# Kernel tuning notes

Hardware: AMD Instinct MI355X
Metric: run time of the kernel (lower is better)

Reference implementation:

```python
import jax, jax.numpy as jnp
import numpy as np

FIELD_DIMS = [26000] * 39
EMBED_DIM = 64
MLP_DIMS = [400, 400, 400]
BATCH = 16384
OFFSETS = jnp.asarray(np.concatenate(([0], np.cumsum(FIELD_DIMS)[:-1])), dtype=jnp.int32)
BN_INV = 1.0 / np.sqrt(1.0 + 1e-5)  # eval-mode BatchNorm1d: running_mean=0, running_var=1


def setup_inputs() -> dict:
    key = jax.random.key(0)
    ks = jax.random.split(key, 16)
    B, F, E = BATCH, len(FIELD_DIMS), EMBED_DIM
    V = sum(FIELD_DIMS)
    s = lambda k, shp, sc=0.05: (jax.random.normal(k, shp, jnp.float32) * sc)
    inp = {
        "x": jax.random.randint(ks[0], (B, F), 0, FIELD_DIMS[0], dtype=jnp.int32),
        "emb_table": s(ks[1], (V, E)),
        "lin_table": s(ks[2], (V, 1)),
        "lin_bias": jnp.zeros((1,), jnp.float32),
        "sparse_var": s(ks[3], (F, E), 0.1),
        "Wt": s(ks[4], (F, E, E)),  # per-field Linear weights, (out,in) layout
        "bt": jnp.zeros((F, E), jnp.float32),
    }
    dims = [F * E] + MLP_DIMS
    for i in range(3):
        inp[f"W{i+1}"] = s(ks[5 + i], (dims[i], dims[i + 1]))
        inp[f"b{i+1}"] = jnp.zeros((dims[i + 1],), jnp.float32)
        inp[f"g{i+1}"] = jnp.ones((dims[i + 1],), jnp.float32)
        inp[f"be{i+1}"] = jnp.zeros((dims[i + 1],), jnp.float32)
    inp["Wout"] = s(ks[9], (MLP_DIMS[-1], 1))
    inp["bout"] = jnp.zeros((1,), jnp.float32)
    return inp


def reference(x, emb_table, lin_table, lin_bias, sparse_var, Wt, bt,
              W1, b1, g1, be1, W2, b2, g2, be2, W3, b3, g3, be3, Wout, bout):
    B = x.shape[0]
    idx = x + OFFSETS[None, :]                       # (B, F) global vocab ids
    # sparse gate (detached in torch), eval-mode hard threshold mask
    sv = jax.nn.sigmoid(jax.lax.stop_gradient(sparse_var) * 15.0)
    sv = jnp.where(sv > 0.001, sv, 0.0)              # (F, E)
    embed_x = emb_table[idx] * sv                    # (B, F, E) gather + gate
    # per-field small Linear, batched as one einsum (torch: y = e @ W.T + b)
    trans = jnp.einsum('bfi,foi->bfo', embed_x, Wt) + bt  # (B, F, E)
    # FM second-order term
    sum_f = trans.sum(axis=1)                        # (B, E)
    fm = 0.5 * jnp.sum(sum_f * sum_f - (trans * trans).sum(axis=1),
                       axis=-1, keepdims=True)       # (B, 1)
    # first-order linear term
    lin = lin_table[idx].sum(axis=1) + lin_bias      # (B, 1)
    # MLP on flattened gated embeddings (Linear -> BN(eval) -> ReLU)
    h = embed_x.reshape(B, -1)
    for W, b, g, be in ((W1, b1, g1, be1), (W2, b2, g2, be2), (W3, b3, g3, be3)):
        h = jax.nn.relu((h @ W + b) * (BN_INV * g) + be)
    mlp = h @ Wout + bout                            # (B, 1)
    return jax.nn.sigmoid(jnp.squeeze(lin + fm + mlp, axis=1))  # (B,)
```

## Files before the change

kernel.cpp:

```cpp
#include <hip/hip_runtime.h>

#define BT 16384
#define NF 39
#define FD 26000

typedef unsigned short u16;
typedef unsigned int u32;
typedef short bf16x8 __attribute__((ext_vector_type(8)));
typedef float f32x4 __attribute__((ext_vector_type(4)));

__device__ __forceinline__ float bf2f(u16 h) {
  union { u32 u; float f; } v; v.u = ((u32)h) << 16; return v.f;
}
__device__ __forceinline__ u16 f2bf(float f) {
  union { float f; u32 u; } v; v.f = f;
  u32 r = v.u + 0x7fffu + ((v.u >> 16) & 1u);
  return (u16)(r >> 16);
}

__device__ __forceinline__ void gld16(const u16* g, u16* l) {
  __builtin_amdgcn_global_load_lds(
      (const __attribute__((address_space(1))) void*)g,
      (__attribute__((address_space(3))) void*)l, 16, 0, 0);
}

__global__ __launch_bounds__(256) void k_embed(
    const int* __restrict__ x, const float* __restrict__ emb,
    const float* __restrict__ lin_table, const float* __restrict__ lin_bias,
    const float* __restrict__ sparse_var, const float* __restrict__ Wt,
    const float* __restrict__ bt, u16* __restrict__ h0, float* __restrict__ base)
{
  __shared__ u16                s_x[32 * NF];
  __shared__ float              s_sv[NF * 64];
  __shared__ float              s_bt[NF * 64];
  __shared__ __align__(16) u16  s_emb[32 * 72];
  __shared__ __align__(16) u16  s_wt[64 * 72];
  __shared__ float              s_S[32 * 65];
  __shared__ float              s_Qp[64];
  __shared__ float              s_lin[32];

  const int tid = threadIdx.x;
  const int b0 = blockIdx.x * 32;

  for (int i = tid; i < 32 * NF; i += 256) s_x[i] = (u16)x[b0 * NF + i];
  for (int i = tid; i < NF * 64; i += 256) {
    float v = sparse_var[i];
    float s = 1.0f / (1.0f + __expf(-15.0f * v));
    s_sv[i] = (s > 0.001f) ? s : 0.0f;
    s_bt[i] = bt[i];
  }
  __syncthreads();

  const int wave = tid >> 6, lane = tid & 63;
  const int quad = lane >> 4, c16 = lane & 15;
  const int mt = wave & 1, nh = wave >> 1;

  float q[4] = {0.f, 0.f, 0.f, 0.f};
  float accS[2][4];
  #pragma unroll
  for (int j = 0; j < 2; ++j)
    #pragma unroll
    for (int r = 0; r < 4; ++r) accS[j][r] = 0.f;

  const int g_row = tid >> 3, g_c8 = (tid & 7) * 8;

  for (int f = 0; f < NF; ++f) {
    #pragma unroll
    for (int it = 0; it < 2; ++it) {
      int row = g_row + it * 32;
      float4 w0 = *(const float4*)&Wt[f * 4096 + row * 64 + g_c8];
      float4 w1 = *(const float4*)&Wt[f * 4096 + row * 64 + g_c8 + 4];
      union { uint4 v; u16 h[8]; } p;
      p.h[0] = f2bf(w0.x); p.h[1] = f2bf(w0.y); p.h[2] = f2bf(w0.z); p.h[3] = f2bf(w0.w);
      p.h[4] = f2bf(w1.x); p.h[5] = f2bf(w1.y); p.h[6] = f2bf(w1.z); p.h[7] = f2bf(w1.w);
      *(uint4*)&s_wt[row * 72 + g_c8] = p.v;
    }
    {
      long gi = (long)((int)s_x[g_row * NF + f] + f * FD);
      float4 e0 = *(const float4*)&emb[gi * 64 + g_c8];
      float4 e1 = *(const float4*)&emb[gi * 64 + g_c8 + 4];
      union { uint4 v; u16 h[8]; } p;
      p.h[0] = f2bf(e0.x * s_sv[f * 64 + g_c8 + 0]);
      p.h[1] = f2bf(e0.y * s_sv[f * 64 + g_c8 + 1]);
      p.h[2] = f2bf(e0.z * s_sv[f * 64 + g_c8 + 2]);
      p.h[3] = f2bf(e0.w * s_sv[f * 64 + g_c8 + 3]);
      p.h[4] = f2bf(e1.x * s_sv[f * 64 + g_c8 + 4]);
      p.h[5] = f2bf(e1.y * s_sv[f * 64 + g_c8 + 5]);
      p.h[6] = f2bf(e1.z * s_sv[f * 64 + g_c8 + 6]);
      p.h[7] = f2bf(e1.w * s_sv[f * 64 + g_c8 + 7]);
      *(uint4*)&s_emb[g_row * 72 + g_c8] = p.v;
      *(uint4*)&h0[(long)(b0 + g_row) * 2496 + f * 64 + g_c8] = p.v;
    }
    __syncthreads();

    bf16x8 a0 = *(const bf16x8*)&s_emb[(mt * 16 + c16) * 72 + quad * 8];
    bf16x8 a1 = *(const bf16x8*)&s_emb[(mt * 16 + c16) * 72 + 32 + quad * 8];
    #pragma unroll
    for (int j = 0; j < 2; ++j) {
      int nt = nh * 2 + j;
      bf16x8 bb0 = *(const bf16x8*)&s_wt[(nt * 16 + c16) * 72 + quad * 8];
      bf16x8 bb1 = *(const bf16x8*)&s_wt[(nt * 16 + c16) * 72 + 32 + quad * 8];
      f32x4 acc = {0.f, 0.f, 0.f, 0.f};
      acc = __builtin_amdgcn_mfma_f32_16x16x32_bf16(a0, bb0, acc, 0, 0, 0);
      acc = __builtin_amdgcn_mfma_f32_16x16x32_bf16(a1, bb1, acc, 0, 0, 0);
      float btv = s_bt[f * 64 + nt * 16 + c16];
      #pragma unroll
      for (int r = 0; r < 4; ++r) {
        float t = acc[r] + btv;
        accS[j][r] += t;
        q[r] += t * t;
      }
    }
    __syncthreads();
  }

  #pragma unroll
  for (int j = 0; j < 2; ++j)
    #pragma unroll
    for (int r = 0; r < 4; ++r)
      s_S[(mt * 16 + quad * 4 + r) * 65 + (nh * 2 + j) * 16 + c16] = accS[j][r];

  #pragma unroll
  for (int r = 0; r < 4; ++r) {
    float v = q[r];
    v += __shfl_xor(v, 1, 64);
    v += __shfl_xor(v, 2, 64);
    v += __shfl_xor(v, 4, 64);
    v += __shfl_xor(v, 8, 64);
    if (c16 == 0) s_Qp[nh * 32 + mt * 16 + quad * 4 + r] = v;
  }

  {
    int row = tid >> 3, fi = tid & 7;
    float lv = 0.f;
    for (int f = fi; f < NF; f += 8)
      lv += lin_table[(int)s_x[row * NF + f] + f * FD];
    lv += __shfl_xor(lv, 1, 64);
    lv += __shfl_xor(lv, 2, 64);
    lv += __shfl_xor(lv, 4, 64);
    if (fi == 0) s_lin[row] = lv;
  }
  __syncthreads();

  if (tid < 32) {
    float s2 = 0.f;
    #pragma unroll 8
    for (int e = 0; e < 64; ++e) { float v = s_S[tid * 65 + e]; s2 += v * v; }
    float fmv = 0.5f * (s2 - (s_Qp[tid] + s_Qp[32 + tid]));
    base[b0 + tid] = s_lin[tid] + lin_bias[0] + fmv;
  }
}

__global__ __launch_bounds__(256) void k_gemm(
    const u16* __restrict__ A, int lda, const u16* __restrict__ Bt, int ldb,
    int kit, const float* __restrict__ bias, const float* __restrict__ g,
    const float* __restrict__ be, u16* __restrict__ C, int ldc)
{
  __shared__ __align__(16) u16 sA[128 * 64];
  __shared__ __align__(16) u16 sB[80 * 64];

  const int tid = threadIdx.x;
  int bid = blockIdx.x;
  int xcd = bid & 7;
  int j = bid >> 3;
  const int m0 = (xcd * 16 + j / 5) * 128;
  const int n0 = (j % 5) * 80;

  const int wave = tid >> 6, lane = tid & 63;
  const int quad = lane >> 4, c16 = lane & 15;

  const int srow = lane >> 3;
  const int sclog = (lane & 7) ^ (srow & 7);
  const u16* gA = A + (long)m0 * lda + sclog * 8;
  const u16* gB = Bt + (long)n0 * ldb + sclog * 8;

  f32x4 acc[2][5];
  #pragma unroll
  for (int mtt = 0; mtt < 2; ++mtt)
    #pragma unroll
    for (int nt = 0; nt < 5; ++nt) acc[mtt][nt] = {0.f, 0.f, 0.f, 0.f};

  for (int kk = 0; kk < kit; ++kk) {
    const int k0 = kk * 64;
    #pragma unroll
    for (int it = 0; it < 4; ++it) {
      int s = wave * 4 + it;
      gld16(gA + (long)(s * 8 + srow) * lda + k0, &sA[s * 512]);
    }
    gld16(gB + (long)(wave * 8 + srow) * ldb + k0, &sB[wave * 512]);
    gld16(gB + (long)((wave + 4) * 8 + srow) * ldb + k0, &sB[(wave + 4) * 512]);
    if (wave < 2)
      gld16(gB + (long)((wave + 8) * 8 + srow) * ldb + k0, &sB[(wave + 8) * 512]);
    __syncthreads();

    #pragma unroll
    for (int ks = 0; ks < 2; ++ks) {
      const int co = ((ks * 4 + quad) ^ (c16 & 7)) * 8;
      bf16x8 a0 = *(const bf16x8*)&sA[(wave * 32 + c16) * 64 + co];
      bf16x8 a1 = *(const bf16x8*)&sA[(wave * 32 + 16 + c16) * 64 + co];
      #pragma unroll
      for (int nt = 0; nt < 5; ++nt) {
        bf16x8 b = *(const bf16x8*)&sB[(nt * 16 + c16) * 64 + co];
        acc[0][nt] = __builtin_amdgcn_mfma_f32_16x16x32_bf16(a0, b, acc[0][nt], 0, 0, 0);
        acc[1][nt] = __builtin_amdgcn_mfma_f32_16x16x32_bf16(a1, b, acc[1][nt], 0, 0, 0);
      }
    }
    __syncthreads();
  }

  const float BN_INV = 0.9999950000374997f;
  #pragma unroll
  for (int nt = 0; nt < 5; ++nt) {
    int col = n0 + nt * 16 + c16;
    float bb = bias[col];
    float sc = BN_INV * g[col];
    float bv = be[col];
    #pragma unroll
    for (int mtt = 0; mtt < 2; ++mtt) {
      #pragma unroll
      for (int r = 0; r < 4; ++r) {
        int row = m0 + wave * 32 + mtt * 16 + quad * 4 + r;
        float y = (acc[mtt][nt][r] + bb) * sc + bv;
        y = fmaxf(y, 0.f);
        C[(long)row * ldc + col] = f2bf(y);
      }
    }
  }
  if (ldc > 400 && n0 == 320) {
    int npad = ldc - 400;
    for (int s = tid; s < 128 * npad; s += 256) {
      int rr = s / npad, cc = s % npad;
      C[(long)(m0 + rr) * ldc + 400 + cc] = 0;
    }
  }
}

__global__ __launch_bounds__(256) void k_transpose3(
    const float* __restrict__ W1, u16* __restrict__ W1T,
    const float* __restrict__ W2, u16* __restrict__ W2T,
    const float* __restrict__ W3, u16* __restrict__ W3T)
{
  int z = blockIdx.z;
  const float* in = (z == 0) ? W1 : (z == 1) ? W2 : W3;
  u16* out = (z == 0) ? W1T : (z == 1) ? W2T : W3T;
  int R = (z == 0) ? 2496 : 400;
  int Rpad = (z == 0) ? 2496 : 448;
  const int C = 400;
  int r0 = blockIdx.y * 32, c0 = blockIdx.x * 32;
  if (r0 >= Rpad) return;
  __shared__ u16 t[32][33];
  int tx = threadIdx.x & 31, ty = threadIdx.x >> 5;
  for (int i = ty; i < 32; i += 8) {
    int r = r0 + i, c = c0 + tx;
    t[i][tx] = (r < R && c < C) ? f2bf(in[(long)r * C + c]) : (u16)0;
  }
  __syncthreads();
  for (int i = ty; i < 32; i += 8) {
    int c = c0 + i, r = r0 + tx;
    if (c < C && r < Rpad) out[(long)c * Rpad + r] = t[tx][i];
  }
}

__global__ __launch_bounds__(256) void k_final(
    const u16* __restrict__ h3, const float* __restrict__ Wout,
    const float* __restrict__ bout, const float* __restrict__ base,
    float* __restrict__ out)
{
  int wave = threadIdx.x >> 6, lane = threadIdx.x & 63;
  int b = blockIdx.x * 4 + wave;
  float s = 0.f;
  for (int jj = lane; jj < 400; jj += 64)
    s += bf2f(h3[(long)b * 448 + jj]) * Wout[jj];
  #pragma unroll
  for (int m = 32; m >= 1; m >>= 1) s += __shfl_xor(s, m, 64);
  if (lane == 0) {
    float z = s + base[b] + bout[0];
    out[b] = 1.0f / (1.0f + __expf(-z));
  }
}

extern "C" void kernel_launch(void* const* d_in, const int* in_sizes, int n_in,
                              void* d_out, int out_size, void* d_ws, size_t ws_size,
                              hipStream_t stream)
{
  const int*   x         = (const int*)d_in[0];
  const float* emb       = (const float*)d_in[1];
  const float* lin_table = (const float*)d_in[2];
  const float* lin_bias  = (const float*)d_in[3];
  const float* svar      = (const float*)d_in[4];
  const float* Wt        = (const float*)d_in[5];
  const float* bt        = (const float*)d_in[6];
  const float* W1  = (const float*)d_in[7];
  const float* b1  = (const float*)d_in[8];
  const float* g1  = (const float*)d_in[9];
  const float* be1 = (const float*)d_in[10];
  const float* W2  = (const float*)d_in[11];
  const float* b2  = (const float*)d_in[12];
  const float* g2  = (const float*)d_in[13];
  const float* be2 = (const float*)d_in[14];
  const float* W3  = (const float*)d_in[15];
  const float* b3  = (const float*)d_in[16];
  const float* g3  = (const float*)d_in[17];
  const float* be3 = (const float*)d_in[18];
  const float* Wo  = (const float*)d_in[19];
  const float* bo  = (const float*)d_in[20];

  char* ws = (char*)d_ws;
  size_t off = 0;
  u16* h0 = (u16*)(ws + off);   off += (size_t)BT * 2496 * 2;
  u16* h1 = (u16*)(ws + off);   off += (size_t)BT * 448 * 2;
  u16* h2 = (u16*)(ws + off);   off += (size_t)BT * 448 * 2;
  u16* h3 = (u16*)(ws + off);   off += (size_t)BT * 448 * 2;
  float* base = (float*)(ws + off); off += (size_t)BT * 4;
  u16* W1T = (u16*)(ws + off);  off += (size_t)400 * 2496 * 2;
  u16* W2T = (u16*)(ws + off);  off += (size_t)400 * 448 * 2;
  u16* W3T = (u16*)(ws + off);  off += (size_t)400 * 448 * 2;
  (void)ws_size; (void)in_sizes; (void)n_in; (void)out_size;

  k_transpose3<<<dim3(13, 78, 3), 256, 0, stream>>>(W1, W1T, W2, W2T, W3, W3T);
  k_embed<<<512, 256, 0, stream>>>(x, emb, lin_table, lin_bias, svar, Wt, bt,
                                   h0, base);
  k_gemm<<<640, 256, 0, stream>>>(h0, 2496, W1T, 2496, 39, b1, g1, be1, h1, 448);
  k_gemm<<<640, 256, 0, stream>>>(h1, 448, W2T, 448, 7, b2, g2, be2, h2, 448);
  k_gemm<<<640, 256, 0, stream>>>(h2, 448, W3T, 448, 7, b3, g3, be3, h3, 448);
  k_final<<<4096, 256, 0, stream>>>(h3, Wo, bo, base, (float*)d_out);
}
```

Before: 480.0 us.

## Precast Wt to bf16 once and double-buffer the per-field embed loop

Adds a prep kernel that converts the per-field weights Wt to bf16 once, alongside the MLP weight transposes. k_embed then streams those weights into swizzled LDS through global_load_lds instead of having every block reload and convert the fp32 weights. The gather for field f+1 and its Wt tile are prefetched into double buffers while the MFMA work for field f runs, which leaves one barrier per field instead of two. The FM reduction is folded into registers and warp shuffles, removing the s_S shared-memory pass. The cost is more LDS, an extra prep pass over Wt, and reliance on the XOR swizzle and async LDS loads being correctly ordered.

```diff
diff --git a/kernel.cpp b/kernel.cpp
--- a/kernel.cpp
+++ b/kernel.cpp
@@ -17,26 +17,55 @@
   u32 r = v.u + 0x7fffu + ((v.u >> 16) & 1u);
   return (u16)(r >> 16);
 }
-
 __device__ __forceinline__ void gld16(const u16* g, u16* l) {
   __builtin_amdgcn_global_load_lds(
       (const __attribute__((address_space(1))) void*)g,
       (__attribute__((address_space(3))) void*)l, 16, 0, 0);
 }
 
+__global__ __launch_bounds__(256) void k_prep(
+    const float* __restrict__ W1, u16* __restrict__ W1T,
+    const float* __restrict__ W2, u16* __restrict__ W2T,
+    const float* __restrict__ W3, u16* __restrict__ W3T,
+    const float* __restrict__ Wt, u16* __restrict__ Wtb)
+{
+  int z = blockIdx.z;
+  if (z == 3) {
+    int idx = (blockIdx.y * 14 + blockIdx.x) * 256 + threadIdx.x;
+    if (idx < NF * 4096) Wtb[idx] = f2bf(Wt[idx]);
+    return;
+  }
+  const float* in = (z == 0) ? W1 : (z == 1) ? W2 : W3;
+  u16* outp = (z == 0) ? W1T : (z == 1) ? W2T : W3T;
+  int K = (z == 0) ? 2496 : 400;
+  int Kpad = (z == 0) ? 2496 : 448;
+  int r0 = blockIdx.y * 32, c0 = blockIdx.x * 32;
+  if (r0 >= Kpad) return;
+  __shared__ u16 t[32][33];
+  int tx = threadIdx.x & 31, ty = threadIdx.x >> 5;
+  for (int i = ty; i < 32; i += 8) {
+    int r = r0 + i, c = c0 + tx;
+    t[i][tx] = (r < K && c < 400) ? f2bf(in[(long)r * 400 + c]) : (u16)0;
+  }
+  __syncthreads();
+  int r = r0 + tx;
+  if (r < Kpad)
+    for (int i = ty; i < 32; i += 8)
+      outp[(long)(c0 + i) * Kpad + r] = t[tx][i];
+}
+
 __global__ __launch_bounds__(256) void k_embed(
     const int* __restrict__ x, const float* __restrict__ emb,
     const float* __restrict__ lin_table, const float* __restrict__ lin_bias,
-    const float* __restrict__ sparse_var, const float* __restrict__ Wt,
+    const float* __restrict__ sparse_var, const u16* __restrict__ Wtb,
     const float* __restrict__ bt, u16* __restrict__ h0, float* __restrict__ base)
 {
   __shared__ u16                s_x[32 * NF];
   __shared__ float              s_sv[NF * 64];
   __shared__ float              s_bt[NF * 64];
-  __shared__ __align__(16) u16  s_emb[32 * 72];
-  __shared__ __align__(16) u16  s_wt[64 * 72];
-  __shared__ float              s_S[32 * 65];
-  __shared__ float              s_Qp[64];
+  __shared__ __align__(16) u16  s_emb[2][32 * 72];
+  __shared__ __align__(16) u16  s_wt[2][64 * 64];
+  __shared__ float              s_fm[64];
   __shared__ float              s_lin[32];
 
   const int tid = threadIdx.x;
@@ -54,56 +83,65 @@
   const int wave = tid >> 6, lane = tid & 63;
   const int quad = lane >> 4, c16 = lane & 15;
   const int mt = wave & 1, nh = wave >> 1;
+  const int g_row = tid >> 3, g_c8 = (tid & 7) * 8;
+  const int wrow = lane >> 3;
+  const int wchk = (lane & 7) ^ wrow;
 
   float q[4] = {0.f, 0.f, 0.f, 0.f};
-  float accS[2][4];
-  #pragma unroll
-  for (int j = 0; j < 2; ++j)
-    #pragma unroll
-    for (int r = 0; r < 4; ++r) accS[j][r] = 0.f;
-
-  const int g_row = tid >> 3, g_c8 = (tid & 7) * 8;
+  float accS[2][4] = {{0.f,0.f,0.f,0.f},{0.f,0.f,0.f,0.f}};
+
+  #pragma unroll
+  for (int i = 0; i < 2; ++i) {
+    int ii = wave * 2 + i;
+    gld16(Wtb + (ii * 8 + wrow) * 64 + wchk * 8, &s_wt[0][ii * 512]);
+  }
+  {
+    long gi = (long)((int)s_x[g_row * NF + 0]);
+    float4 e0 = *(const float4*)&emb[gi * 64 + g_c8];
+    float4 e1 = *(const float4*)&emb[gi * 64 + g_c8 + 4];
+    union { uint4 v; u16 h[8]; } p;
+    p.h[0] = f2bf(e0.x * s_sv[g_c8 + 0]);
+    p.h[1] = f2bf(e0.y * s_sv[g_c8 + 1]);
+    p.h[2] = f2bf(e0.z * s_sv[g_c8 + 2]);
+    p.h[3] = f2bf(e0.w * s_sv[g_c8 + 3]);
+    p.h[4] = f2bf(e1.x * s_sv[g_c8 + 4]);
+    p.h[5] = f2bf(e1.y * s_sv[g_c8 + 5]);
+    p.h[6] = f2bf(e1.z * s_sv[g_c8 + 6]);
+    p.h[7] = f2bf(e1.w * s_sv[g_c8 + 7]);
+    *(uint4*)&s_emb[0][g_row * 72 + g_c8] = p.v;
+    *(uint4*)&h0[(long)(b0 + g_row) * 2496 + g_c8] = p.v;
+  }
+  __syncthreads();
 
   for (int f = 0; f < NF; ++f) {
-    #pragma unroll
-    for (int it = 0; it < 2; ++it) {
-      int row = g_row + it * 32;
-      float4 w0 = *(const float4*)&Wt[f * 4096 + row * 64 + g_c8];
-      float4 w1 = *(const float4*)&Wt[f * 4096 + row * 64 + g_c8 + 4];
-      union { uint4 v; u16 h[8]; } p;
-      p.h[0] = f2bf(w0.x); p.h[1] = f2bf(w0.y); p.h[2] = f2bf(w0.z); p.h[3] = f2bf(w0.w);
-      p.h[4] = f2bf(w1.x); p.h[5] = f2bf(w1.y); p.h[6] = f2bf(w1.z); p.h[7] = f2bf(w1.w);
-      *(uint4*)&s_wt[row * 72 + g_c8] = p.v;
-    }
-    {
-      long gi = (long)((int)s_x[g_row * NF + f] + f * FD);
-      float4 e0 = *(const float4*)&emb[gi * 64 + g_c8];
-      float4 e1 = *(const float4*)&emb[gi * 64 + g_c8 + 4];
-      union { uint4 v; u16 h[8]; } p;
-      p.h[0] = f2bf(e0.x * s_sv[f * 64 + g_c8 + 0]);
-      p.h[1] = f2bf(e0.y * s_sv[f * 64 + g_c8 + 1]);
-      p.h[2] = f2bf(e0.z * s_sv[f * 64 + g_c8 + 2]);
-      p.h[3] = f2bf(e0.w * s_sv[f * 64 + g_c8 + 3]);
-      p.h[4] = f2bf(e1.x * s_sv[f * 64 + g_c8 + 4]);
-      p.h[5] = f2bf(e1.y * s_sv[f * 64 + g_c8 + 5]);
-      p.h[6] = f2bf(e1.z * s_sv[f * 64 + g_c8 + 6]);
-      p.h[7] = f2bf(e1.w * s_sv[f * 64 + g_c8 + 7]);
-      *(uint4*)&s_emb[g_row * 72 + g_c8] = p.v;
-      *(uint4*)&h0[(long)(b0 + g_row) * 2496 + f * 64 + g_c8] = p.v;
-    }
-    __syncthreads();
-
-    bf16x8 a0 = *(const bf16x8*)&s_emb[(mt * 16 + c16) * 72 + quad * 8];
-    bf16x8 a1 = *(const bf16x8*)&s_emb[(mt * 16 + c16) * 72 + 32 + quad * 8];
+    const int cur = f & 1, nxt = cur ^ 1;
+    float4 e0, e1;
+    const bool more = (f + 1) < NF;
+    if (more) {
+      #pragma unroll
+      for (int i = 0; i < 2; ++i) {
+        int ii = wave * 2 + i;
+        gld16(Wtb + (f + 1) * 4096 + (ii * 8 + wrow) * 64 + wchk * 8,
+              &s_wt[nxt][ii * 512]);
+      }
+      long gi = (long)((int)s_x[g_row * NF + f + 1] + (f + 1) * FD);
+      e0 = *(const float4*)&emb[gi * 64 + g_c8];
+      e1 = *(const float4*)&emb[gi * 64 + g_c8 + 4];
+    }
+
+    bf16x8 a0 = *(const bf16x8*)&s_emb[cur][(mt * 16 + c16) * 72 + quad * 8];
+    bf16x8 a1 = *(const bf16x8*)&s_emb[cur][(mt * 16 + c16) * 72 + 32 + quad * 8];
     #pragma unroll
     for (int j = 0; j < 2; ++j) {
-      int nt = nh * 2 + j;
-      bf16x8 bb0 = *(const bf16x8*)&s_wt[(nt * 16 + c16) * 72 + quad * 8];
-      bf16x8 bb1 = *(const bf16x8*)&s_wt[(nt * 16 + c16) * 72 + 32 + quad * 8];
+      int row = (nh * 2 + j) * 16 + c16;
+      int pc0 = quad ^ (row & 7);
+      int pc1 = (quad + 4) ^ (row & 7);
+      bf16x8 bb0 = *(const bf16x8*)&s_wt[cur][row * 64 + pc0 * 8];
+      bf16x8 bb1 = *(const bf16x8*)&s_wt[cur][row * 64 + pc1 * 8];
       f32x4 acc = {0.f, 0.f, 0.f, 0.f};
       acc = __builtin_amdgcn_mfma_f32_16x16x32_bf16(a0, bb0, acc, 0, 0, 0);
       acc = __builtin_amdgcn_mfma_f32_16x16x32_bf16(a1, bb1, acc, 0, 0, 0);
-      float btv = s_bt[f * 64 + nt * 16 + c16];
+      float btv = s_bt[f * 64 + row];
       #pragma unroll
       for (int r = 0; r < 4; ++r) {
         float t = acc[r] + btv;
@@ -111,25 +149,33 @@
         q[r] += t * t;
       }
     }
+
+    if (more) {
+      union { uint4 v; u16 h[8]; } p;
+      const float* sv = &s_sv[(f + 1) * 64 + g_c8];
+      p.h[0] = f2bf(e0.x * sv[0]);
+      p.h[1] = f2bf(e0.y * sv[1]);
+      p.h[2] = f2bf(e0.z * sv[2]);
+      p.h[3] = f2bf(e0.w * sv[3]);
+      p.h[4] = f2bf(e1.x * sv[4]);
+      p.h[5] = f2bf(e1.y * sv[5]);
+      p.h[6] = f2bf(e1.z * sv[6]);
+      p.h[7] = f2bf(e1.w * sv[7]);
+      *(uint4*)&s_emb[nxt][g_row * 72 + g_c8] = p.v;
+      *(uint4*)&h0[(long)(b0 + g_row) * 2496 + (f + 1) * 64 + g_c8] = p.v;
+    }
     __syncthreads();
   }
 
   #pragma unroll
-  for (int j = 0; j < 2; ++j)
-    #pragma unroll
-    for (int r = 0; r < 4; ++r)
-      s_S[(mt * 16 + quad * 4 + r) * 65 + (nh * 2 + j) * 16 + c16] = accS[j][r];
-
-  #pragma unroll
   for (int r = 0; r < 4; ++r) {
-    float v = q[r];
+    float v = accS[0][r] * accS[0][r] + accS[1][r] * accS[1][r] - q[r];
     v += __shfl_xor(v, 1, 64);
     v += __shfl_xor(v, 2, 64);
     v += __shfl_xor(v, 4, 64);
     v += __shfl_xor(v, 8, 64);
-    if (c16 == 0) s_Qp[nh * 32 + mt * 16 + quad * 4 + r] = v;
-  }
-
+    if (c16 == 0) s_fm[nh * 32 + mt * 16 + quad * 4 + r] = v;
+  }
   {
     int row = tid >> 3, fi = tid & 7;
     float lv = 0.f;
@@ -141,14 +187,9 @@
     if (fi == 0) s_lin[row] = lv;
   }
   __syncthreads();
-
-  if (tid < 32) {
-    float s2 = 0.f;
-    #pragma unroll 8
-    for (int e = 0; e < 64; ++e) { float v = s_S[tid * 65 + e]; s2 += v * v; }
-    float fmv = 0.5f * (s2 - (s_Qp[tid] + s_Qp[32 + tid]));
-    base[b0 + tid] = s_lin[tid] + lin_bias[0] + fmv;
-  }
+  if (tid < 32)
+    base[b0 + tid] = s_lin[tid] + lin_bias[0]
+                   + 0.5f * (s_fm[tid] + s_fm[32 + tid]);
 }
 
 __global__ __launch_bounds__(256) void k_gemm(
@@ -232,32 +273,6 @@
       int rr = s / npad, cc = s % npad;
       C[(long)(m0 + rr) * ldc + 400 + cc] = 0;
     }
-  }
-}
-
-__global__ __launch_bounds__(256) void k_transpose3(
-    const float* __restrict__ W1, u16* __restrict__ W1T,
-    const float* __restrict__ W2, u16* __restrict__ W2T,
-    const float* __restrict__ W3, u16* __restrict__ W3T)
-{
-  int z = blockIdx.z;
-  const float* in = (z == 0) ? W1 : (z == 1) ? W2 : W3;
-  u16* out = (z == 0) ? W1T : (z == 1) ? W2T : W3T;
-  int R = (z == 0) ? 2496 : 400;
-  int Rpad = (z == 0) ? 2496 : 448;
-  const int C = 400;
-  int r0 = blockIdx.y * 32, c0 = blockIdx.x * 32;
-  if (r0 >= Rpad) return;
-  __shared__ u16 t[32][33];
-  int tx = threadIdx.x & 31, ty = threadIdx.x >> 5;
-  for (int i = ty; i < 32; i += 8) {
-    int r = r0 + i, c = c0 + tx;
-    t[i][tx] = (r < R && c < C) ? f2bf(in[(long)r * C + c]) : (u16)0;
-  }
-  __syncthreads();
-  for (int i = ty; i < 32; i += 8) {
-    int c = c0 + i, r = r0 + tx;
-    if (c < C && r < Rpad) out[(long)c * Rpad + r] = t[tx][i];
   }
 }
 
@@ -307,18 +322,19 @@
 
   char* ws = (char*)d_ws;
   size_t off = 0;
-  u16* h0 = (u16*)(ws + off);   off += (size_t)BT * 2496 * 2;
-  u16* h1 = (u16*)(ws + off);   off += (size_t)BT * 448 * 2;
-  u16* h2 = (u16*)(ws + off);   off += (size_t)BT * 448 * 2;
-  u16* h3 = (u16*)(ws + off);   off += (size_t)BT * 448 * 2;
+  u16* h0 = (u16*)(ws + off);     off += (size_t)BT * 2496 * 2;
+  u16* h1 = (u16*)(ws + off);     off += (size_t)BT * 448 * 2;
+  u16* h2 = (u16*)(ws + off);     off += (size_t)BT * 448 * 2;
+  u16* h3 = (u16*)(ws + off);     off += (size_t)BT * 448 * 2;
   float* base = (float*)(ws + off); off += (size_t)BT * 4;
-  u16* W1T = (u16*)(ws + off);  off += (size_t)400 * 2496 * 2;
-  u16* W2T = (u16*)(ws + off);  off += (size_t)400 * 448 * 2;
-  u16* W3T = (u16*)(ws + off);  off += (size_t)400 * 448 * 2;
+  u16* W1T = (u16*)(ws + off);    off += (size_t)448 * 2496 * 2;
+  u16* W2T = (u16*)(ws + off);    off += (size_t)448 * 448 * 2;
+  u16* W3T = (u16*)(ws + off);    off += (size_t)448 * 448 * 2;
+  u16* Wtb = (u16*)(ws + off);    off += (size_t)NF * 4096 * 2;
   (void)ws_size; (void)in_sizes; (void)n_in; (void)out_size;
 
-  k_transpose3<<<dim3(13, 78, 3), 256, 0, stream>>>(W1, W1T, W2, W2T, W3, W3T);
-  k_embed<<<512, 256, 0, stream>>>(x, emb, lin_table, lin_bias, svar, Wt, bt,
+  k_prep<<<dim3(14, 78, 4), 256, 0, stream>>>(W1, W1T, W2, W2T, W3, W3T, Wt, Wtb);
+  k_embed<<<512, 256, 0, stream>>>(x, emb, lin_table, lin_bias, svar, Wtb, bt,
                                    h0, base);
   k_gemm<<<640, 256, 0, stream>>>(h0, 2496, W1T, 2496, 39, b1, g1, be1, h1, 448);
   k_gemm<<<640, 256, 0, stream>>>(h1, 448, W2T, 448, 7, b2, g2, be2, h2, 448);
```

New measurement: 474.7 us. Within noise of the previous version (-1.1%).
